# Kernel optimization log

Measured on AMD Instinct MI355X. Metric: run time of the kernel, lower is better.

The kernel has to match this reference:

```python
import jax, jax.numpy as jnp
import numpy as np

B, L, D, H, HD, K, MAXLEN = 4, 2048, 1024, 16, 64, 32, 2048


def setup_inputs() -> dict:
    key = jax.random.key(0)
    ks = jax.random.split(key, 8)
    s = 0.02  # init scale (stand-in for lecun-normal magnitude)
    return {
        "inputs_q": jax.random.normal(ks[0], (B, L, D), jnp.float32),
        "inputs_kv": jax.random.normal(ks[1], (B, L, D), jnp.float32),
        "Wv": jax.random.normal(ks[2], (D, H, HD), jnp.float32) * s,   # value DenseGeneral kernel
        "bv": jnp.zeros((H, HD), jnp.float32),                          # value bias
        "r1": jax.random.normal(ks[3], (H, MAXLEN, K), jnp.float32) * s,  # param 'random1'
        "r2": jax.random.normal(ks[4], (H, K, MAXLEN), jnp.float32) * s,  # param 'random2'
        "Wo": jax.random.normal(ks[5], (H, HD, D), jnp.float32) * s,   # output DenseGeneral kernel
        "bo": jnp.zeros((D,), jnp.float32),                             # output bias
    }


def reference(inputs_q, inputs_kv, Wv, bv, r1, r2, Wo, bo):
    # SynthesizerAttention with ignore_dot_product=True, mode='factorized_random',
    # no masks, deterministic (no dropout).
    qlen = inputs_q.shape[-2]
    kvlen = inputs_kv.shape[-2]
    # value projection: [B, Lkv, H, HD]; key=value, query=inputs_q (unused for scores)
    v = jnp.einsum('bnd,dhk->bnhk', inputs_kv, Wv) + bv
    # factorized random synthetic scores: [H, Lq, Lkv]
    syn = jnp.einsum('hlk,hkn->hln', r1[:, :qlen, :], r2[:, :, :kvlen])
    # softmax over the key/value axis (norm_dims in synthetic_attention).
    # Scores are batch-independent, so softmax once per head (broadcast over B).
    attn = jax.nn.softmax(syn, axis=-1)
    # weighted sum over values: [B, Lq, H, HD]
    y = jnp.einsum('hln,bnhk->blhk', attn, v)
    # output projection over (H, HD): [B, Lq, D]
    return jnp.einsum('blhk,hkd->bld', y, Wo) + bo
```

## Files before the change

### kernel.cpp

```cpp
#include <hip/hip_runtime.h>
#include <hip/hip_bf16.h>

#define LL 2048

typedef __bf16 bf16x8 __attribute__((ext_vector_type(8)));
typedef __bf16 bf16x4 __attribute__((ext_vector_type(4)));
typedef float f32x4 __attribute__((ext_vector_type(4)));

__device__ inline void gl_lds16(const __bf16* g, __bf16* l) {
    __builtin_amdgcn_global_load_lds((const __attribute__((address_space(1))) void*)g,
                                     (__attribute__((address_space(3))) void*)l, 16, 0, 0);
}

__global__ __launch_bounds__(256) void prep(const float* __restrict__ inputs_kv,
                                            const float* __restrict__ r1,
                                            const float* __restrict__ Wv,
                                            const float* __restrict__ Wo,
                                            const float* __restrict__ r2,
                                            __bf16* __restrict__ A1,
                                            __bf16* __restrict__ r1b,
                                            __bf16* __restrict__ Wvt,
                                            __bf16* __restrict__ Wot,
                                            __bf16* __restrict__ r2t) {
    __shared__ float Ls[32][65];
    int bid = blockIdx.x;
    const int tid = threadIdx.x;
    if (bid < 4608) {
        const float* in = (bid < 4096) ? inputs_kv : r1;
        __bf16* out = (bid < 4096) ? A1 : r1b;
        const int t = ((bid < 4096) ? bid : bid - 4096) * 256 + tid;
        const float4* in4 = (const float4*)in;
        float4 f0 = in4[t * 2], f1 = in4[t * 2 + 1];
        bf16x8 o;
        o[0] = (__bf16)f0.x; o[1] = (__bf16)f0.y; o[2] = (__bf16)f0.z; o[3] = (__bf16)f0.w;
        o[4] = (__bf16)f1.x; o[5] = (__bf16)f1.y; o[6] = (__bf16)f1.z; o[7] = (__bf16)f1.w;
        *(bf16x8*)&out[(size_t)t * 8] = o;
        return;
    }
    bid -= 4608;
    const float* in;
    __bf16* out;
    int R, C, r0, c0;
    if (bid < 512) {
        in = Wv; out = Wvt; R = 1024; C = 1024;
        c0 = (bid & 15) * 64; r0 = (bid >> 4) * 32;
    } else if (bid < 1024) {
        bid -= 512;
        in = Wo; out = Wot; R = 1024; C = 1024;
        c0 = (bid & 15) * 64; r0 = (bid >> 4) * 32;
    } else {
        bid -= 1024;
        const int bz = bid >> 5;
        in = r2 + (size_t)bz * 65536; out = r2t + (size_t)bz * 65536;
        R = 32; C = 2048;
        c0 = (bid & 31) * 64; r0 = 0;
    }
#pragma unroll
    for (int p = 0; p < 2; ++p) {
        int f = tid + 256 * p;
        int row = f >> 4, c4 = (f & 15) << 2;
        float4 v = *(const float4*)&in[(size_t)(r0 + row) * C + c0 + c4];
        Ls[row][c4 + 0] = v.x; Ls[row][c4 + 1] = v.y;
        Ls[row][c4 + 2] = v.z; Ls[row][c4 + 3] = v.w;
    }
    __syncthreads();
    const int orow = tid >> 2, rc = (tid & 3) << 3;
    bf16x8 o;
#pragma unroll
    for (int j = 0; j < 8; ++j) o[j] = (__bf16)Ls[rc + j][orow];
    *(bf16x8*)&out[(size_t)(c0 + orow) * R + r0 + rc] = o;
}

template <int MODE>
__global__ __launch_bounds__(256) void gemm_bt(const __bf16* __restrict__ A,
                                               const __bf16* __restrict__ Bt,
                                               const float* __restrict__ bias,
                                               void* __restrict__ Cout,
                                               int M, int N, int K) {
    __shared__ alignas(16) __bf16 As[128 * 32];
    __shared__ alignas(16) __bf16 Bs[128 * 32];
    const int tid = threadIdx.x;
    const int lane = tid & 63;
    const int wid = __builtin_amdgcn_readfirstlane(tid >> 6);
    const int row0 = blockIdx.y * 128, col0 = blockIdx.x * 128;
    const int l15 = lane & 15, quad = lane >> 4;
    const int wr = wid & 1, wc = wid >> 1;
    const int s0 = wid * 2, s1 = s0 + 1;

    const __bf16* ga0 = A + (size_t)(row0 + s0 * 16 + (lane >> 2)) * K + ((lane & 3) << 3);
    const __bf16* ga1 = ga0 + (size_t)16 * K;
    const __bf16* gb0 = Bt + (size_t)(col0 + s0 * 16 + (lane >> 2)) * K + ((lane & 3) << 3);
    const __bf16* gb1 = gb0 + (size_t)16 * K;
    __bf16* la0 = As + s0 * 512;
    __bf16* la1 = As + s1 * 512;
    __bf16* lb0 = Bs + s0 * 512;
    __bf16* lb1 = Bs + s1 * 512;

    f32x4 acc[4][4];
#pragma unroll
    for (int i = 0; i < 4; ++i)
#pragma unroll
        for (int j = 0; j < 4; ++j) acc[i][j] = (f32x4){0.f, 0.f, 0.f, 0.f};

    for (int k0 = 0; k0 < K; k0 += 32) {
        __syncthreads();
        gl_lds16(ga0 + k0, la0);
        gl_lds16(ga1 + k0, la1);
        gl_lds16(gb0 + k0, lb0);
        gl_lds16(gb1 + k0, lb1);
        __syncthreads();
        bf16x8 af[4], bfv[4];
#pragma unroll
        for (int i = 0; i < 4; ++i)
            af[i] = *(const bf16x8*)&As[(wr * 64 + i * 16 + l15) * 32 + quad * 8];
#pragma unroll
        for (int j = 0; j < 4; ++j)
            bfv[j] = *(const bf16x8*)&Bs[(wc * 64 + j * 16 + l15) * 32 + quad * 8];
#pragma unroll
        for (int i = 0; i < 4; ++i)
#pragma unroll
            for (int j = 0; j < 4; ++j)
                acc[i][j] = __builtin_amdgcn_mfma_f32_16x16x32_bf16(af[i], bfv[j], acc[i][j], 0, 0, 0);
    }

#pragma unroll
    for (int i = 0; i < 4; ++i) {
        const int rg = row0 + wr * 64 + i * 16 + quad * 4;
#pragma unroll
        for (int j = 0; j < 4; ++j) {
            const int cg = col0 + wc * 64 + j * 16 + l15;
            const float bb = bias[cg];
            if (MODE == 0) {
                const int b = rg >> 11, n = rg & 2047;
                const int h = cg >> 6, hd = cg & 63;
                const int nc = n >> 6, ks = (n >> 5) & 1, qj = (n >> 3) & 3, j0 = n & 7;
                const int jt = hd >> 4, fl = hd & 15;
                __bf16* V3 = (__bf16*)Cout;
                bf16x4 v;
#pragma unroll
                for (int r = 0; r < 4; ++r) v[r] = (__bf16)(acc[i][j][r] + bb);
                *(bf16x4*)&V3[(size_t)(((h * 32 + nc) * 4 + b) * 4096) +
                              (jt * 2 + ks) * 512 + fl * 32 + qj * 8 + j0] = v;
            } else {
                float* Cf = (float*)Cout;
#pragma unroll
                for (int r = 0; r < 4; ++r)
                    Cf[(size_t)(rg + r) * N + cg] = acc[i][j][r] + bb;
            }
        }
    }
}

__global__ __launch_bounds__(512) void attn_pv_v4(const __bf16* __restrict__ r1b,
                                                  const __bf16* __restrict__ r2t,
                                                  const __bf16* __restrict__ V3,
                                                  __bf16* __restrict__ yb) {
    __shared__ alignas(16) __bf16 Ps[2 * 2 * 4 * 1024];
    const int tid = threadIdx.x;
    const int lane = tid & 63;
    const int w = __builtin_amdgcn_readfirstlane(tid >> 6);
    const int b = w & 3, lh = w >> 2;
    const int l15 = lane & 15, quad = lane >> 4;
    const int id = blockIdx.x;
    const int h = id & 15;
    const int l0 = (id >> 4) << 7;

    bf16x8 bf1[4];
#pragma unroll
    for (int i = 0; i < 4; ++i)
        bf1[i] = *(const bf16x8*)&r1b[(size_t)(h * 2048 + l0 + lh * 64 + i * 16 + l15) * 32 + quad * 8];

    const __bf16* r2p = r2t + (size_t)(h * 2048 + b * 16 + l15) * 32 + quad * 8;
    const __bf16* vp = V3 + (size_t)((h * 32) * 4 + b) * 4096 + l15 * 32 + quad * 8;

    bf16x8 r2f = *(const bf16x8*)r2p;
    bf16x8 vpf[4][2];
#pragma unroll
    for (int jt = 0; jt < 4; ++jt)
#pragma unroll
        for (int ks = 0; ks < 2; ++ks)
            vpf[jt][ks] = *(const bf16x8*)(vp + (jt * 2 + ks) * 512);

    bf16x8 ones;
#pragma unroll
    for (int e = 0; e < 8; ++e) ones[e] = (__bf16)1.0f;

    f32x4 acc[4][4];
    f32x4 den[4];
#pragma unroll
    for (int i = 0; i < 4; ++i) {
        den[i] = (f32x4){0.f, 0.f, 0.f, 0.f};
#pragma unroll
        for (int j = 0; j < 4; ++j) acc[i][j] = (f32x4){0.f, 0.f, 0.f, 0.f};
    }
    const f32x4 zero4 = {0.f, 0.f, 0.f, 0.f};

    const int kw = b >> 1;
    const int jg = (b & 1) * 2 + (quad >> 1);
    const int q4 = (quad & 1) * 4;

    for (int c = 0; c < 32; ++c) {
        const int cn = (c < 31) ? 1 : 0;
        f32x4 s[4];
#pragma unroll
        for (int i = 0; i < 4; ++i)
            s[i] = __builtin_amdgcn_mfma_f32_16x16x32_bf16(r2f, bf1[i], zero4, 0, 0, 0);
        r2f = *(const bf16x8*)(r2p + (size_t)cn * 2048);
        __bf16* ps = &Ps[((c & 1) * 2 + lh) * 4096];
#pragma unroll
        for (int i = 0; i < 4; ++i) {
            bf16x4 p4;
#pragma unroll
            for (int r = 0; r < 4; ++r) p4[r] = (__bf16)__expf(s[i][r]);
            *(bf16x4*)&ps[i * 1024 + kw * 512 + l15 * 32 + jg * 8 + q4] = p4;
        }
        __syncthreads();
        bf16x8 pa[4][2];
#pragma unroll
        for (int i = 0; i < 4; ++i)
#pragma unroll
            for (int ks = 0; ks < 2; ++ks)
                pa[i][ks] = *(const bf16x8*)&ps[i * 1024 + ks * 512 + l15 * 32 + quad * 8];
#pragma unroll
        for (int ks = 0; ks < 2; ++ks) {
#pragma unroll
            for (int i = 0; i < 4; ++i) {
#pragma unroll
                for (int jt = 0; jt < 4; ++jt)
                    acc[i][jt] = __builtin_amdgcn_mfma_f32_16x16x32_bf16(pa[i][ks], vpf[jt][ks],
                                                                         acc[i][jt], 0, 0, 0);
                den[i] = __builtin_amdgcn_mfma_f32_16x16x32_bf16(pa[i][ks], ones, den[i], 0, 0, 0);
            }
        }
        vp += cn * 16384;
#pragma unroll
        for (int jt = 0; jt < 4; ++jt)
#pragma unroll
            for (int ks = 0; ks < 2; ++ks)
                vpf[jt][ks] = *(const bf16x8*)(vp + (jt * 2 + ks) * 512);
    }

#pragma unroll
    for (int i = 0; i < 4; ++i) {
#pragma unroll
        for (int r = 0; r < 4; ++r) {
            const float iv = 1.0f / den[i][r];
            const int l = l0 + lh * 64 + i * 16 + quad * 4 + r;
            const size_t rowbase = ((size_t)b * LL + l) * 1024 + h * 64;
#pragma unroll
            for (int jt = 0; jt < 4; ++jt)
                yb[rowbase + jt * 16 + l15] = (__bf16)(acc[i][jt][r] * iv);
        }
    }
}

extern "C" void kernel_launch(void* const* d_in, const int* in_sizes, int n_in,
                              void* d_out, int out_size, void* d_ws, size_t ws_size,
                              hipStream_t stream) {
    const float* inputs_kv = (const float*)d_in[1];
    const float* Wv = (const float*)d_in[2];
    const float* bv = (const float*)d_in[3];
    const float* r1 = (const float*)d_in[4];
    const float* r2 = (const float*)d_in[5];
    const float* Wo = (const float*)d_in[6];
    const float* bo = (const float*)d_in[7];
    float* out = (float*)d_out;

    char* ws = (char*)d_ws;
    const size_t MB = 1024 * 1024;
    __bf16* A1  = (__bf16*)(ws);
    __bf16* Wvt = (__bf16*)(ws + 16 * MB);
    __bf16* Wot = (__bf16*)(ws + 18 * MB);
    __bf16* r1b = (__bf16*)(ws + 20 * MB);
    __bf16* r2t = (__bf16*)(ws + 22 * MB);
    __bf16* V3  = (__bf16*)(ws + 24 * MB);
    __bf16* yb  = (__bf16*)(ws + 40 * MB);

    prep<<<6144, 256, 0, stream>>>(inputs_kv, r1, Wv, Wo, r2, A1, r1b, Wvt, Wot, r2t);
    gemm_bt<0><<<dim3(8, 64), 256, 0, stream>>>(A1, Wvt, bv, V3, 8192, 1024, 1024);
    attn_pv_v4<<<256, 512, 0, stream>>>(r1b, r2t, V3, yb);
    gemm_bt<1><<<dim3(8, 64), 256, 0, stream>>>(yb, Wot, bo, out, 8192, 1024, 1024);
}
```

Baseline: 220.7 us.

## Fuse fp32-to-bf16 input conversion into value GEMM and pad P tile in LDS

The separate prep pass that converted inputs_kv (32 MB fp32) to bf16 is removed. The value-projection GEMM now loads fp32 A directly, converts it in registers and stores it to LDS, which saves a full write and re-read of a 16 MB intermediate. The attention kernel's P tile in LDS is padded to a row stride of 40 to cut bank conflicts, and the r2 prefetch index now wraps modulo 32. In exchange, the GEMM's A path becomes synchronous register loads instead of async global-to-LDS copies, so less of the load latency may be hidden.

```diff
diff --git a/kernel.cpp b/kernel.cpp
--- a/kernel.cpp
+++ b/kernel.cpp
@@ -12,12 +12,17 @@
                                      (__attribute__((address_space(3))) void*)l, 16, 0, 0);
 }
 
-__global__ __launch_bounds__(256) void prep(const float* __restrict__ inputs_kv,
-                                            const float* __restrict__ r1,
+__device__ inline bf16x8 cvt2bf8(float4 a, float4 b) {
+    bf16x8 o;
+    o[0] = (__bf16)a.x; o[1] = (__bf16)a.y; o[2] = (__bf16)a.z; o[3] = (__bf16)a.w;
+    o[4] = (__bf16)b.x; o[5] = (__bf16)b.y; o[6] = (__bf16)b.z; o[7] = (__bf16)b.w;
+    return o;
+}
+
+__global__ __launch_bounds__(256) void prep(const float* __restrict__ r1,
                                             const float* __restrict__ Wv,
                                             const float* __restrict__ Wo,
                                             const float* __restrict__ r2,
-                                            __bf16* __restrict__ A1,
                                             __bf16* __restrict__ r1b,
                                             __bf16* __restrict__ Wvt,
                                             __bf16* __restrict__ Wot,
@@ -25,19 +30,13 @@
     __shared__ float Ls[32][65];
     int bid = blockIdx.x;
     const int tid = threadIdx.x;
-    if (bid < 4608) {
-        const float* in = (bid < 4096) ? inputs_kv : r1;
-        __bf16* out = (bid < 4096) ? A1 : r1b;
-        const int t = ((bid < 4096) ? bid : bid - 4096) * 256 + tid;
-        const float4* in4 = (const float4*)in;
-        float4 f0 = in4[t * 2], f1 = in4[t * 2 + 1];
-        bf16x8 o;
-        o[0] = (__bf16)f0.x; o[1] = (__bf16)f0.y; o[2] = (__bf16)f0.z; o[3] = (__bf16)f0.w;
-        o[4] = (__bf16)f1.x; o[5] = (__bf16)f1.y; o[6] = (__bf16)f1.z; o[7] = (__bf16)f1.w;
-        *(bf16x8*)&out[(size_t)t * 8] = o;
+    if (bid < 512) {
+        const int t = bid * 256 + tid;
+        const float4* in4 = (const float4*)r1;
+        *(bf16x8*)&r1b[(size_t)t * 8] = cvt2bf8(in4[t * 2], in4[t * 2 + 1]);
         return;
     }
-    bid -= 4608;
+    bid -= 512;
     const float* in;
     __bf16* out;
     int R, C, r0, c0;
@@ -71,11 +70,88 @@
     *(bf16x8*)&out[(size_t)(c0 + orow) * R + r0 + rc] = o;
 }
 
-template <int MODE>
+__global__ __launch_bounds__(256) void gemm_af32(const float* __restrict__ A,
+                                                 const __bf16* __restrict__ Bt,
+                                                 const float* __restrict__ bias,
+                                                 __bf16* __restrict__ V3,
+                                                 int M, int N, int K) {
+    __shared__ alignas(16) __bf16 As[128 * 32];
+    __shared__ alignas(16) __bf16 Bs[128 * 32];
+    const int tid = threadIdx.x;
+    const int lane = tid & 63;
+    const int wid = __builtin_amdgcn_readfirstlane(tid >> 6);
+    const int row0 = blockIdx.y * 128, col0 = blockIdx.x * 128;
+    const int l15 = lane & 15, quad = lane >> 4;
+    const int wr = wid & 1, wc = wid >> 1;
+    const int s0 = wid * 2, s1 = s0 + 1;
+
+    const int arow = s0 * 16 + (lane >> 2);
+    const int k8 = (lane & 3) << 3;
+    const float* gaf0 = A + (size_t)(row0 + arow) * K + k8;
+    const float* gaf1 = gaf0 + (size_t)16 * K;
+    __bf16* lwa0 = As + arow * 32 + k8;
+    __bf16* lwa1 = lwa0 + 16 * 32;
+
+    const __bf16* gb0 = Bt + (size_t)(col0 + s0 * 16 + (lane >> 2)) * K + k8;
+    const __bf16* gb1 = gb0 + (size_t)16 * K;
+    __bf16* lb0 = Bs + s0 * 512;
+    __bf16* lb1 = Bs + s1 * 512;
+
+    f32x4 acc[4][4];
+#pragma unroll
+    for (int i = 0; i < 4; ++i)
+#pragma unroll
+        for (int j = 0; j < 4; ++j) acc[i][j] = (f32x4){0.f, 0.f, 0.f, 0.f};
+
+    for (int k0 = 0; k0 < K; k0 += 32) {
+        __syncthreads();
+        gl_lds16(gb0 + k0, lb0);
+        gl_lds16(gb1 + k0, lb1);
+        float4 a0 = *(const float4*)(gaf0 + k0);
+        float4 a1 = *(const float4*)(gaf0 + k0 + 4);
+        float4 a2 = *(const float4*)(gaf1 + k0);
+        float4 a3 = *(const float4*)(gaf1 + k0 + 4);
+        *(bf16x8*)lwa0 = cvt2bf8(a0, a1);
+        *(bf16x8*)lwa1 = cvt2bf8(a2, a3);
+        __syncthreads();
+        bf16x8 af[4], bfv[4];
+#pragma unroll
+        for (int i = 0; i < 4; ++i)
+            af[i] = *(const bf16x8*)&As[(wr * 64 + i * 16 + l15) * 32 + quad * 8];
+#pragma unroll
+        for (int j = 0; j < 4; ++j)
+            bfv[j] = *(const bf16x8*)&Bs[(wc * 64 + j * 16 + l15) * 32 + quad * 8];
+#pragma unroll
+        for (int i = 0; i < 4; ++i)
+#pragma unroll
+            for (int j = 0; j < 4; ++j)
+                acc[i][j] = __builtin_amdgcn_mfma_f32_16x16x32_bf16(af[i], bfv[j], acc[i][j], 0, 0, 0);
+    }
+
+#pragma unroll
+    for (int i = 0; i < 4; ++i) {
+        const int rg = row0 + wr * 64 + i * 16 + quad * 4;
+#pragma unroll
+        for (int j = 0; j < 4; ++j) {
+            const int cg = col0 + wc * 64 + j * 16 + l15;
+            const float bb = bias[cg];
+            const int b = rg >> 11, n = rg & 2047;
+            const int h = cg >> 6, hd = cg & 63;
+            const int nc = n >> 6, ks = (n >> 5) & 1, qj = (n >> 3) & 3, j0 = n & 7;
+            const int jt = hd >> 4, fl = hd & 15;
+            bf16x4 v;
+#pragma unroll
+            for (int r = 0; r < 4; ++r) v[r] = (__bf16)(acc[i][j][r] + bb);
+            *(bf16x4*)&V3[(size_t)(((h * 32 + nc) * 4 + b) * 4096) +
+                          (jt * 2 + ks) * 512 + fl * 32 + qj * 8 + j0] = v;
+        }
+    }
+}
+
 __global__ __launch_bounds__(256) void gemm_bt(const __bf16* __restrict__ A,
                                                const __bf16* __restrict__ Bt,
                                                const float* __restrict__ bias,
-                                               void* __restrict__ Cout,
+                                               float* __restrict__ Cf,
                                                int M, int N, int K) {
     __shared__ alignas(16) __bf16 As[128 * 32];
     __shared__ alignas(16) __bf16 Bs[128 * 32];
@@ -130,32 +206,18 @@
         for (int j = 0; j < 4; ++j) {
             const int cg = col0 + wc * 64 + j * 16 + l15;
             const float bb = bias[cg];
-            if (MODE == 0) {
-                const int b = rg >> 11, n = rg & 2047;
-                const int h = cg >> 6, hd = cg & 63;
-                const int nc = n >> 6, ks = (n >> 5) & 1, qj = (n >> 3) & 3, j0 = n & 7;
-                const int jt = hd >> 4, fl = hd & 15;
-                __bf16* V3 = (__bf16*)Cout;
-                bf16x4 v;
-#pragma unroll
-                for (int r = 0; r < 4; ++r) v[r] = (__bf16)(acc[i][j][r] + bb);
-                *(bf16x4*)&V3[(size_t)(((h * 32 + nc) * 4 + b) * 4096) +
-                              (jt * 2 + ks) * 512 + fl * 32 + qj * 8 + j0] = v;
-            } else {
-                float* Cf = (float*)Cout;
-#pragma unroll
-                for (int r = 0; r < 4; ++r)
-                    Cf[(size_t)(rg + r) * N + cg] = acc[i][j][r] + bb;
-            }
-        }
-    }
-}
-
-__global__ __launch_bounds__(512) void attn_pv_v4(const __bf16* __restrict__ r1b,
+#pragma unroll
+            for (int r = 0; r < 4; ++r)
+                Cf[(size_t)(rg + r) * N + cg] = acc[i][j][r] + bb;
+        }
+    }
+}
+
+__global__ __launch_bounds__(512) void attn_pv_v6(const __bf16* __restrict__ r1b,
                                                   const __bf16* __restrict__ r2t,
                                                   const __bf16* __restrict__ V3,
                                                   __bf16* __restrict__ yb) {
-    __shared__ alignas(16) __bf16 Ps[2 * 2 * 4 * 1024];
+    __shared__ alignas(16) __bf16 Ps[4 * 5120];
     const int tid = threadIdx.x;
     const int lane = tid & 63;
     const int w = __builtin_amdgcn_readfirstlane(tid >> 6);
@@ -201,18 +263,19 @@
 
     for (int c = 0; c < 32; ++c) {
         const int cn = (c < 31) ? 1 : 0;
+        const int nx = (c + 1) & 31;
         f32x4 s[4];
 #pragma unroll
         for (int i = 0; i < 4; ++i)
             s[i] = __builtin_amdgcn_mfma_f32_16x16x32_bf16(r2f, bf1[i], zero4, 0, 0, 0);
-        r2f = *(const bf16x8*)(r2p + (size_t)cn * 2048);
-        __bf16* ps = &Ps[((c & 1) * 2 + lh) * 4096];
+        r2f = *(const bf16x8*)(r2p + (size_t)nx * 2048);
+        __bf16* ps = &Ps[((c & 1) * 2 + lh) * 5120];
 #pragma unroll
         for (int i = 0; i < 4; ++i) {
             bf16x4 p4;
 #pragma unroll
             for (int r = 0; r < 4; ++r) p4[r] = (__bf16)__expf(s[i][r]);
-            *(bf16x4*)&ps[i * 1024 + kw * 512 + l15 * 32 + jg * 8 + q4] = p4;
+            *(bf16x4*)&ps[((i * 2 + kw) * 16 + l15) * 40 + jg * 8 + q4] = p4;
         }
         __syncthreads();
         bf16x8 pa[4][2];
@@ -220,7 +283,7 @@
         for (int i = 0; i < 4; ++i)
 #pragma unroll
             for (int ks = 0; ks < 2; ++ks)
-                pa[i][ks] = *(const bf16x8*)&ps[i * 1024 + ks * 512 + l15 * 32 + quad * 8];
+                pa[i][ks] = *(const bf16x8*)&ps[((i * 2 + ks) * 16 + l15) * 40 + quad * 8];
 #pragma unroll
         for (int ks = 0; ks < 2; ++ks) {
 #pragma unroll
@@ -268,16 +331,15 @@
 
     char* ws = (char*)d_ws;
     const size_t MB = 1024 * 1024;
-    __bf16* A1  = (__bf16*)(ws);
-    __bf16* Wvt = (__bf16*)(ws + 16 * MB);
-    __bf16* Wot = (__bf16*)(ws + 18 * MB);
-    __bf16* r1b = (__bf16*)(ws + 20 * MB);
-    __bf16* r2t = (__bf16*)(ws + 22 * MB);
-    __bf16* V3  = (__bf16*)(ws + 24 * MB);
-    __bf16* yb  = (__bf16*)(ws + 40 * MB);
-
-    prep<<<6144, 256, 0, stream>>>(inputs_kv, r1, Wv, Wo, r2, A1, r1b, Wvt, Wot, r2t);
-    gemm_bt<0><<<dim3(8, 64), 256, 0, stream>>>(A1, Wvt, bv, V3, 8192, 1024, 1024);
-    attn_pv_v4<<<256, 512, 0, stream>>>(r1b, r2t, V3, yb);
-    gemm_bt<1><<<dim3(8, 64), 256, 0, stream>>>(yb, Wot, bo, out, 8192, 1024, 1024);
-}
+    __bf16* Wvt = (__bf16*)(ws);
+    __bf16* Wot = (__bf16*)(ws + 2 * MB);
+    __bf16* r1b = (__bf16*)(ws + 4 * MB);
+    __bf16* r2t = (__bf16*)(ws + 6 * MB);
+    __bf16* V3  = (__bf16*)(ws + 8 * MB);
+    __bf16* yb  = (__bf16*)(ws + 24 * MB);
+
+    prep<<<2048, 256, 0, stream>>>(r1, Wv, Wo, r2, r1b, Wvt, Wot, r2t);
+    gemm_af32<<<dim3(8, 64), 256, 0, stream>>>(inputs_kv, Wvt, bv, V3, 8192, 1024, 1024);
+    attn_pv_v6<<<256, 512, 0, stream>>>(r1b, r2t, V3, yb);
+    gemm_bt<<<dim3(8, 64), 256, 0, stream>>>(yb, Wot, bo, out, 8192, 1024, 1024);
+}
```

After: 234.4 us. 6.2% more time.
